# Kernel tuning notes

Measured on AMD Instinct MI355X. Metric: run time of the kernel, lower is better.

## Reference

```python
import jax, jax.numpy as jnp
import numpy as np

B, T, N = 64, 128, 64   # batch, win_size, input_size (= node_num)
H, E, K, CS = 64, 128, 7, 8  # hidden_size, embed_size, kernel_size, control_size
NEG_SLOPE = 0.2


def _p(key, shape, scale=0.05):
    return scale * jax.random.normal(key, shape, dtype=jnp.float32)


def setup_inputs() -> dict:
    key = jax.random.key(0)
    ks = jax.random.split(key, 32)
    inp = {
        "x": jax.random.normal(ks[0], (B, T, N), dtype=jnp.float32),
        "y": jax.random.normal(ks[1], (B, T, CS), dtype=jnp.float32),
        # Conv1d(N -> N, kernel K)
        "conv_w": _p(ks[2], (N, N, K)),
        "conv_b": _p(ks[3], (N,)),
        # rnn_enc GRU: input N -> hidden H
        "We_ih": _p(ks[4], (3 * H, N)), "We_hh": _p(ks[5], (3 * H, H)),
        "be_ih": _p(ks[6], (3 * H,)), "be_hh": _p(ks[7], (3 * H,)),
        # MP_GAT linears
        "Ww": _p(ks[8], (E, 2 * T)), "bw": _p(ks[9], (E,)),
        "Wa": _p(ks[10], (1, E)), "ba": _p(ks[11], (1,)),
        # encoder GRU: input H+N -> H
        "Wm_ih": _p(ks[12], (3 * H, H + N)), "Wm_hh": _p(ks[13], (3 * H, H)),
        "bm_ih": _p(ks[14], (3 * H,)), "bm_hh": _p(ks[15], (3 * H,)),
        # rnn_dec GRU: input H -> H
        "Wd_ih": _p(ks[16], (3 * H, H)), "Wd_hh": _p(ks[17], (3 * H, H)),
        "bd_ih": _p(ks[18], (3 * H,)), "bd_hh": _p(ks[19], (3 * H,)),
        # fc_dec: H -> N
        "W_dec": _p(ks[20], (N, H)), "b_dec": _p(ks[21], (N,)),
        # fc_pred: Linear(H,N), ReLU, Linear(N,N)
        "W_p1": _p(ks[22], (N, H)), "b_p1": _p(ks[23], (N,)),
        "W_p2": _p(ks[24], (N, N)), "b_p2": _p(ks[25], (N,)),
    }
    return inp


def gru_seq(x_seq, Wih, Whh, bih, bhh):
    """torch nn.GRU (batch_first, h0=0). x_seq: [B,T,in] -> [B,T,H]."""
    gi = jnp.einsum('bti,gi->btg', x_seq, Wih) + bih  # [B,T,3H] (precompute input proj)
    h0 = jnp.zeros((x_seq.shape[0], Whh.shape[1]), x_seq.dtype)

    def step(h, gi_t):
        gh = h @ Whh.T + bhh
        i_r, i_z, i_n = jnp.split(gi_t, 3, axis=-1)
        h_r, h_z, h_n = jnp.split(gh, 3, axis=-1)
        r = jax.nn.sigmoid(i_r + h_r)
        z = jax.nn.sigmoid(i_z + h_z)
        n = jnp.tanh(i_n + r * h_n)
        h_new = (1.0 - z) * n + z * h
        return h_new, h_new

    _, hs = jax.lax.scan(step, h0, jnp.swapaxes(gi, 0, 1))
    return jnp.swapaxes(hs, 0, 1)


def _forward(x, y, conv_w, conv_b, We_ih, We_hh, be_ih, be_hh, Ww, bw, Wa, ba,
             Wm_ih, Wm_hh, bm_ih, bm_hh, Wd_ih, Wd_hh, bd_ih, bd_hh,
             W_dec, b_dec, W_p1, b_p1, W_p2, b_p2):
    # ---- CNN: pad 'same' + Conv1d + SELU. x: [B,T,N] -> channels first [B,N,T]
    pad = (K - 1) // 2
    xc = jnp.swapaxes(x, 1, 2)
    c = jax.lax.conv_general_dilated(xc, conv_w, (1,), [(pad, pad)],
                                     dimension_numbers=('NCH', 'OIH', 'NCH'))
    c = jax.nn.selu(c + conv_b[None, :, None])  # [B,N,T]
    c_btn = jnp.swapaxes(c, 1, 2)               # [B,T,N]

    # ---- rnn_enc GRU over time
    h_out = gru_seq(c_btn, We_ih, We_hh, be_ih, be_hh)  # [B,T,H]

    # ---- MP_GAT on c (v: [B, node, seq] = [B,N,T])
    v = c
    vi = jnp.broadcast_to(v[:, :, None, :], (B, N, N, T))
    vj = jnp.broadcast_to(v[:, None, :, :], (B, N, N, T))
    v_cat = jnp.concatenate([vi, vj], axis=-1)          # [B,N,N,2T]
    x_w = jax.nn.leaky_relu(jnp.einsum('bijt,et->bije', v_cat, Ww) + bw, NEG_SLOPE)
    e = (jnp.einsum('bije,oe->bijo', x_w, Wa) + ba)[..., 0]  # [B,N,N]
    attention = jax.nn.softmax(e, axis=2)
    # dropout is identity in eval mode
    h_mp = jax.nn.sigmoid(jnp.einsum('bij,bjt->bit', attention, v))  # [B,N,T]
    h_mp = jnp.swapaxes(h_mp, 1, 2)                      # [B,T,N]

    # ---- encoder / decoder GRUs (dropout = identity in eval)
    h_cat = jnp.concatenate([h_out, h_mp], axis=2)       # [B,T,H+N]
    h_enc = gru_seq(h_cat, Wm_ih, Wm_hh, bm_ih, bm_hh)
    h_dec = gru_seq(h_enc, Wd_ih, Wd_hh, bd_ih, bd_hh)

    recon = h_dec @ W_dec.T + b_dec                      # [B,T,N]
    p = jax.nn.relu(h_dec[:, 0, :] @ W_p1.T + b_p1)
    pred = p @ W_p2.T + b_p2                             # [B,N]
    return recon, pred


def reference(x, y, conv_w, conv_b, We_ih, We_hh, be_ih, be_hh, Ww, bw, Wa, ba,
              Wm_ih, Wm_hh, bm_ih, bm_hh, Wd_ih, Wd_hh, bd_ih, bd_hh,
              W_dec, b_dec, W_p1, b_p1, W_p2, b_p2):
    return _forward(x, y, conv_w, conv_b, We_ih, We_hh, be_ih, be_hh, Ww, bw, Wa, ba,
                    Wm_ih, Wm_hh, bm_ih, bm_hh, Wd_ih, Wd_hh, bd_ih, bd_hh,
                    W_dec, b_dec, W_p1, b_p1, W_p2, b_p2)
```

## Files before the change

### kernel.cpp

```cpp
#include <hip/hip_runtime.h>
#include <math.h>

#define BB 64
#define TT 128
#define NN 64
#define HH 64
#define EE 128
#define KK 7
#define GG 192

typedef _Float16 half2_t __attribute__((ext_vector_type(2)));

__device__ __forceinline__ float sigmoidf_(float x){ return 1.f/(1.f+expf(-x)); }
__device__ __forceinline__ float fsig_(float x){
  return __builtin_amdgcn_rcpf(1.f + __builtin_amdgcn_exp2f(-1.44269504f * x));
}
__device__ __forceinline__ float ftanh_(float x){
  return fmaf(-2.f, __builtin_amdgcn_rcpf(1.f + __builtin_amdgcn_exp2f(2.88539008f * x)), 1.f);
}

#define PIPE_BARRIER() asm volatile("s_waitcnt lgkmcnt(0)\ns_barrier" ::: "memory")
#define LGKM0() asm volatile("s_waitcnt lgkmcnt(0)" ::: "memory")

__device__ __forceinline__ void loadrow_(float* d, const float* src){
  const float4* p = (const float4*)src;
  #pragma unroll
  for (int i = 0; i < 16; ++i) {
    float4 v = p[i];
    d[4*i] = v.x; d[4*i+1] = v.y; d[4*i+2] = v.z; d[4*i+3] = v.w;
  }
}
__device__ __forceinline__ void loadroww_(half2_t* d, const float* src){
  const float4* p = (const float4*)src;
  #pragma unroll
  for (int i = 0; i < 16; ++i) {
    float4 v = p[i];
    d[2*i]   = half2_t{(_Float16)v.x, (_Float16)v.y};
    d[2*i+1] = half2_t{(_Float16)v.z, (_Float16)v.w};
  }
}
__device__ __forceinline__ void load_h16_(const _Float16* hs, half2_t* hp){
  const float4* s4 = (const float4*)hs;
  #pragma unroll
  for (int j = 0; j < 8; ++j) {
    float4 v = s4[j];
    const half2_t* q = (const half2_t*)&v;
    hp[4*j] = q[0]; hp[4*j+1] = q[1]; hp[4*j+2] = q[2]; hp[4*j+3] = q[3];
  }
}
__device__ __forceinline__ void mvdot3_(const half2_t* hp, const half2_t* w0,
                                        const half2_t* w1, const half2_t* w2,
                                        float& a0, float& a1, float& a2){
  #pragma unroll
  for (int i = 0; i < 32; ++i) {
    a0 = __builtin_amdgcn_fdot2(hp[i], w0[i], a0, false);
    a1 = __builtin_amdgcn_fdot2(hp[i], w1[i], a1, false);
    a2 = __builtin_amdgcn_fdot2(hp[i], w2[i], a2, false);
  }
}

__global__ void conv_s12_kernel(const float* __restrict__ x, const float* __restrict__ w,
                                const float* __restrict__ bias, const float* __restrict__ Ww,
                                float* __restrict__ c_nt, float* __restrict__ c_btn,
                                float* __restrict__ s1, float* __restrict__ s2) {
  const int og = blockIdx.x, b = blockIdx.y, t = threadIdx.x;
  const int o0 = og * 8;
  __shared__ __align__(16) float xs[NN][TT + 1];
  __shared__ __align__(16) float ws[NN * KK][8];
  __shared__ __align__(16) float cs[8][TT];
  for (int idx = t; idx < TT * NN; idx += 128) {
    int tt = idx >> 6, nn = idx & 63;
    xs[nn][tt] = x[(size_t)(b * TT + tt) * NN + nn];
  }
  for (int idx = t; idx < NN * KK * 8; idx += 128) {
    int oo = idx & 7, ik = idx >> 3;
    ws[ik][oo] = w[(size_t)(o0 + oo) * (NN * KK) + ik];
  }
  __syncthreads();
  float acc[8];
  #pragma unroll
  for (int oo = 0; oo < 8; ++oo) acc[oo] = bias[o0 + oo];
  for (int i = 0; i < NN; ++i) {
    #pragma unroll
    for (int k = 0; k < KK; ++k) {
      int tt = t + k - 3;
      if (tt >= 0 && tt < TT) {
        float xv = xs[i][tt];
        const float* wp = &ws[i * KK + k][0];
        float4 w0 = *(const float4*)wp;
        float4 w1 = *(const float4*)(wp + 4);
        acc[0] += xv * w0.x; acc[1] += xv * w0.y; acc[2] += xv * w0.z; acc[3] += xv * w0.w;
        acc[4] += xv * w1.x; acc[5] += xv * w1.y; acc[6] += xv * w1.z; acc[7] += xv * w1.w;
      }
    }
  }
  const float alpha = 1.6732632423543772f, scale = 1.0507009873554805f;
  #pragma unroll
  for (int oo = 0; oo < 8; ++oo) {
    float a = acc[oo];
    float r = a > 0.f ? scale * a : scale * alpha * expm1f(a);
    int o = o0 + oo;
    c_nt[((size_t)b * NN + o) * TT + t] = r;
    c_btn[((size_t)b * TT + t) * NN + o] = r;
    cs[oo][t] = r;
  }
  __syncthreads();
  const float* w1 = Ww + (size_t)t * (2 * TT);
  const float* w2 = w1 + TT;
  float a1[8], a2l[8];
  #pragma unroll
  for (int r = 0; r < 8; ++r) { a1[r] = 0.f; a2l[r] = 0.f; }
  #pragma unroll 2
  for (int k = 0; k < TT; k += 4) {
    float4 wv1 = *(const float4*)(w1 + k);
    float4 wv2 = *(const float4*)(w2 + k);
    #pragma unroll
    for (int r = 0; r < 8; ++r) {
      float4 cv = *(const float4*)&cs[r][k];
      a1[r]  += cv.x * wv1.x + cv.y * wv1.y + cv.z * wv1.z + cv.w * wv1.w;
      a2l[r] += cv.x * wv2.x + cv.y * wv2.y + cv.z * wv2.z + cv.w * wv2.w;
    }
  }
  #pragma unroll
  for (int r = 0; r < 8; ++r) {
    s1[((size_t)b * NN + o0 + r) * EE + t] = a1[r];
    s2[((size_t)b * NN + o0 + r) * EE + t] = a2l[r];
  }
}

__global__ __launch_bounds__(512)
void gat_kernel(const float* __restrict__ s1, const float* __restrict__ s2,
                const float* __restrict__ bw, const float* __restrict__ Wa,
                const float* __restrict__ ba, const float* __restrict__ c_nt,
                float* __restrict__ hmp) {
  const int it = blockIdx.x, b = blockIdx.y, tid = threadIdx.x;
  const int i0 = it * 16;
  __shared__ float s2s[NN][EE + 1];
  __shared__ float s1b[16][EE];
  __shared__ float cs[NN][TT + 1];
  __shared__ float was[EE];
  __shared__ float att[16][NN + 1];
  for (int idx = tid; idx < NN * EE; idx += 512) {
    int j = idx >> 7, e = idx & 127;
    s2s[j][e] = s2[((size_t)b * NN + j) * EE + e] + bw[e];
  }
  for (int idx = tid; idx < 16 * EE; idx += 512) {
    int r = idx >> 7, e = idx & 127;
    s1b[r][e] = s1[((size_t)b * NN + i0 + r) * EE + e];
  }
  for (int idx = tid; idx < NN * TT; idx += 512) {
    int j = idx >> 7, t = idx & 127;
    cs[j][t] = c_nt[((size_t)b * NN + j) * TT + t];
  }
  if (tid < EE) was[tid] = Wa[tid];
  __syncthreads();
  const int wv = tid >> 6, j = tid & 63;
  #pragma unroll
  for (int pass = 0; pass < 2; ++pass) {
    const int il = pass * 8 + wv;
    float acc = 0.f;
    #pragma unroll 8
    for (int e = 0; e < EE; ++e) {
      float v = s1b[il][e] + s2s[j][e];
      v = v > 0.f ? v : 0.2f * v;
      acc += was[e] * v;
    }
    float ej = acc + ba[0];
    float mx = ej;
    for (int off = 32; off >= 1; off >>= 1) mx = fmaxf(mx, __shfl_xor(mx, off));
    float ex = __builtin_amdgcn_exp2f(1.44269504f * (ej - mx));
    float sm = ex;
    for (int off = 32; off >= 1; off >>= 1) sm += __shfl_xor(sm, off);
    att[il][j] = ex / sm;
  }
  __syncthreads();
  for (int o = tid; o < 16 * TT; o += 512) {
    int il = o & 15, t = o >> 4;
    float acc = 0.f;
    #pragma unroll 8
    for (int jj = 0; jj < NN; ++jj) acc += att[il][jj] * cs[jj][t];
    hmp[((size_t)b * TT + t) * NN + i0 + il] = sigmoidf_(acc);
  }
}

__global__ __launch_bounds__(512, 1)
void fused_chain8(const float* __restrict__ c_btn, const float* __restrict__ hmp,
                  const float* __restrict__ We_ih, const float* __restrict__ be_ih,
                  const float* __restrict__ We_hh, const float* __restrict__ be_hh,
                  const float* __restrict__ Wm_ih, const float* __restrict__ bm_ih,
                  const float* __restrict__ Wm_hh, const float* __restrict__ bm_hh,
                  const float* __restrict__ Wd_ih, const float* __restrict__ bd_ih,
                  const float* __restrict__ Wd_hh, const float* __restrict__ bd_hh,
                  const float* __restrict__ W_dec, const float* __restrict__ b_dec,
                  const float* __restrict__ W_p1, const float* __restrict__ b_p1,
                  const float* __restrict__ W_p2, const float* __restrict__ b_p2,
                  float* __restrict__ recon, float* __restrict__ pred) {
  const int b = blockIdx.x, tid = threadIdx.x, wid = tid >> 6, g = tid & 63;
  __shared__ __align__(16) _Float16 cbuf[2][HH], mbuf[2][HH];
  __shared__ __align__(16) _Float16 h1h[2][HH], h2h[2][HH], h3h[2][HH];
  __shared__ __align__(16) float h3f[2][HH];
  __shared__ __align__(16) float q1[2][GG], q2a[2][GG], q2b[2][GG], q3[2][GG];
  __shared__ __align__(16) float h0s[HH], ps[HH];

  half2_t wa[32], wb[32], wc[32];
  float wdec[64];
  float b0 = 0.f, b1 = 0.f, b2 = 0.f;
  float e0 = 0.f, e1 = 0.f, e2 = 0.f;
  if (wid == 0) {
    loadroww_(wa, We_hh + (size_t)g * HH);
    loadroww_(wb, We_hh + (size_t)(g + 64) * HH);
    loadroww_(wc, We_hh + (size_t)(g + 128) * HH);
    b0 = be_hh[g]; b1 = be_hh[64 + g]; b2 = be_hh[128 + g];
  } else if (wid == 1) {
    loadroww_(wa, Wm_hh + (size_t)g * HH);
    loadroww_(wb, Wm_hh + (size_t)(g + 64) * HH);
    loadroww_(wc, Wm_hh + (size_t)(g + 128) * HH);
    b0 = bm_hh[g]; b1 = bm_hh[64 + g]; b2 = bm_hh[128 + g];
  } else if (wid == 2) {
    loadroww_(wa, Wd_hh + (size_t)g * HH);
    loadroww_(wb, Wd_hh + (size_t)(g + 64) * HH);
    loadroww_(wc, Wd_hh + (size_t)(g + 128) * HH);
    b0 = bd_hh[g]; b1 = bd_hh[64 + g]; b2 = bd_hh[128 + g];
    e0 = bd_ih[g]; e1 = bd_ih[64 + g]; e2 = bd_ih[128 + g];
  } else if (wid == 3) {
    loadrow_(wdec, W_dec + (size_t)g * HH);
    b0 = b_dec[g];
  } else if (wid == 4) {
    loadroww_(wa, Wm_ih + (size_t)g * 128);
    loadroww_(wb, Wm_ih + (size_t)(g + 64) * 128);
    loadroww_(wc, Wm_ih + (size_t)(g + 128) * 128);
  } else if (wid == 5) {
    loadroww_(wa, Wd_ih + (size_t)g * HH);
    loadroww_(wb, Wd_ih + (size_t)(g + 64) * HH);
    loadroww_(wc, Wd_ih + (size_t)(g + 128) * HH);
  } else if (wid == 6) {
    loadroww_(wa, We_ih + (size_t)g * HH);
    loadroww_(wb, We_ih + (size_t)(g + 64) * HH);
    loadroww_(wc, We_ih + (size_t)(g + 128) * HH);
    b0 = be_ih[g]; b1 = be_ih[64 + g]; b2 = be_ih[128 + g];
  } else {
    loadroww_(wa, Wm_ih + (size_t)g * 128 + 64);
    loadroww_(wb, Wm_ih + (size_t)(g + 64) * 128 + 64);
    loadroww_(wc, Wm_ih + (size_t)(g + 128) * 128 + 64);
    b0 = bm_ih[g]; b1 = bm_ih[64 + g]; b2 = bm_ih[128 + g];
  }

  if (wid == 0) {
    h1h[0][g] = (_Float16)0.f; h1h[1][g] = (_Float16)0.f;
    h2h[0][g] = (_Float16)0.f; h2h[1][g] = (_Float16)0.f;
    h3h[0][g] = (_Float16)0.f; h3h[1][g] = (_Float16)0.f;
  }
  const float* cb = c_btn + (size_t)b * TT * NN + g;
  const float* hm = hmp   + (size_t)b * TT * NN + g;
  float pf0 = 0.f, pf1 = 0.f;
  if (wid == 6) {
    cbuf[0][g] = (_Float16)cb[0]; cbuf[1][g] = (_Float16)cb[NN];
    pf0 = cb[2 * NN]; pf1 = cb[3 * NN];
  }
  if (wid == 7) {
    mbuf[0][g] = (_Float16)hm[0]; mbuf[1][g] = (_Float16)hm[NN];
    pf0 = hm[2 * NN]; pf1 = hm[3 * NN];
  }
  if (wid <= 2) __builtin_amdgcn_s_setprio(1);
  __syncthreads();

  float hown = 0.f;
  for (int ph = 0; ph < TT + 6; ++ph) {
    const int pw = ph & 1, pr = pw ^ 1;
    if (wid == 6) {
      int t = ph;
      if (t < TT) {
        half2_t hp[32]; load_h16_(&cbuf[pw][0], hp);
        if (t + 2 < TT) cbuf[pw][g] = (_Float16)(pw ? pf1 : pf0);
        float a0 = b0, a1 = b1, a2 = b2;
        if (t + 4 < TT) { float nv = cb[(size_t)(t + 4) * NN]; if (pw) pf1 = nv; else pf0 = nv; }
        mvdot3_(hp, wa, wb, wc, a0, a1, a2);
        q1[pw][g] = a0; q1[pw][64 + g] = a1; q1[pw][128 + g] = a2;
      }
    } else if (wid == 0) {
      int t = ph - 1;
      if (t >= 0 && t < TT) {
        half2_t hp[32]; load_h16_(&h1h[pr][0], hp);
        float a0 = b0, a1 = b1, a2 = b2;
        mvdot3_(hp, wa, wb, wc, a0, a1, a2);
        float r = fsig_(q1[pr][g] + a0), z = fsig_(q1[pr][64 + g] + a1);
        float n = ftanh_(q1[pr][128 + g] + r * a2);
        hown = fmaf(z, hown - n, n);
        h1h[pw][g] = (_Float16)hown;
      }
    } else if (wid == 4) {
      int t = ph - 2;
      if (t >= 0 && t < TT) {
        half2_t hp[32]; load_h16_(&h1h[pr][0], hp);
        float a0 = 0.f, a1 = 0.f, a2 = 0.f;
        mvdot3_(hp, wa, wb, wc, a0, a1, a2);
        q2a[pw][g] = a0; q2a[pw][64 + g] = a1; q2a[pw][128 + g] = a2;
      }
    } else if (wid == 7) {
      int t = ph - 2;
      if (t >= 0 && t < TT) {
        half2_t hp[32]; load_h16_(&mbuf[pw][0], hp);
        if (t + 2 < TT) mbuf[pw][g] = (_Float16)(pw ? pf1 : pf0);
        float a0 = b0, a1 = b1, a2 = b2;
        if (t + 4 < TT) { float nv = hm[(size_t)(t + 4) * NN]; if (pw) pf1 = nv; else pf0 = nv; }
        mvdot3_(hp, wa, wb, wc, a0, a1, a2);
        q2b[pw][g] = a0; q2b[pw][64 + g] = a1; q2b[pw][128 + g] = a2;
      }
    } else if (wid == 1) {
      int t = ph - 3;
      if (t >= 0 && t < TT) {
        half2_t hp[32]; load_h16_(&h2h[pr][0], hp);
        float a0 = b0, a1 = b1, a2 = b2;
        mvdot3_(hp, wa, wb, wc, a0, a1, a2);
        float gr = q2a[pr][g] + q2b[pr][g];
        float gz = q2a[pr][64 + g] + q2b[pr][64 + g];
        float gn = q2a[pr][128 + g] + q2b[pr][128 + g];
        float r = fsig_(gr + a0), z = fsig_(gz + a1), n = ftanh_(gn + r * a2);
        hown = fmaf(z, hown - n, n);
        h2h[pw][g] = (_Float16)hown;
      }
    } else if (wid == 5) {
      int t = ph - 4;
      if (t >= 0 && t < TT) {
        half2_t hp[32]; load_h16_(&h2h[pr][0], hp);
        float a0 = 0.f, a1 = 0.f, a2 = 0.f;
        mvdot3_(hp, wa, wb, wc, a0, a1, a2);
        q3[pw][g] = a0; q3[pw][64 + g] = a1; q3[pw][128 + g] = a2;
      }
    } else if (wid == 2) {
      int t = ph - 5;
      if (t >= 0 && t < TT) {
        half2_t hp[32]; load_h16_(&h3h[pr][0], hp);
        float a0 = b0, a1 = b1, a2 = b2;
        mvdot3_(hp, wa, wb, wc, a0, a1, a2);
        float r = fsig_(q3[pr][g] + e0 + a0), z = fsig_(q3[pr][64 + g] + e1 + a1);
        float n = ftanh_(q3[pr][128 + g] + e2 + r * a2);
        hown = fmaf(z, hown - n, n);
        h3h[pw][g] = (_Float16)hown;
        h3f[pw][g] = hown;
        if (t == 0) h0s[g] = hown;
      }
    } else {
      int t = ph - 6;
      if (t >= 0) {
        const float4* h4 = (const float4*)&h3f[pr][0];
        float a0 = b0, a1 = 0.f;
        #pragma unroll
        for (int i = 0; i < 8; ++i) {
          float4 hv = h4[2 * i], hw = h4[2 * i + 1];
          a0 = fmaf(hv.x, wdec[8*i],   fmaf(hv.y, wdec[8*i+1], fmaf(hv.z, wdec[8*i+2], fmaf(hv.w, wdec[8*i+3], a0))));
          a1 = fmaf(hw.x, wdec[8*i+4], fmaf(hw.y, wdec[8*i+5], fmaf(hw.z, wdec[8*i+6], fmaf(hw.w, wdec[8*i+7], a1))));
        }
        recon[((size_t)b * TT + t) * NN + g] = a0 + a1;
      }
    }
    PIPE_BARRIER();
  }

  if (wid == 0) {
    float w1r[64]; loadrow_(w1r, W_p1 + (size_t)g * HH);
    const float4* h4 = (const float4*)&h0s[0];
    float a = b_p1[g];
    #pragma unroll
    for (int i = 0; i < 16; ++i) {
      float4 hv = h4[i];
      a = fmaf(hv.x, w1r[4*i], fmaf(hv.y, w1r[4*i+1], fmaf(hv.z, w1r[4*i+2], fmaf(hv.w, w1r[4*i+3], a))));
    }
    ps[g] = fmaxf(a, 0.f);
    LGKM0();
    float w2r[64]; loadrow_(w2r, W_p2 + (size_t)g * HH);
    const float4* p4 = (const float4*)&ps[0];
    float c2 = b_p2[g];
    #pragma unroll
    for (int i = 0; i < 16; ++i) {
      float4 pv = p4[i];
      c2 = fmaf(pv.x, w2r[4*i], fmaf(pv.y, w2r[4*i+1], fmaf(pv.z, w2r[4*i+2], fmaf(pv.w, w2r[4*i+3], c2))));
    }
    pred[(size_t)b * NN + g] = c2;
  }
}

extern "C" void kernel_launch(void* const* d_in, const int* in_sizes, int n_in,
                              void* d_out, int out_size, void* d_ws, size_t ws_size,
                              hipStream_t stream) {
  const float* x      = (const float*)d_in[0];
  const float* conv_w = (const float*)d_in[2];
  const float* conv_b = (const float*)d_in[3];
  const float* We_ih  = (const float*)d_in[4];
  const float* We_hh  = (const float*)d_in[5];
  const float* be_ih  = (const float*)d_in[6];
  const float* be_hh  = (const float*)d_in[7];
  const float* Ww     = (const float*)d_in[8];
  const float* bw     = (const float*)d_in[9];
  const float* Wa     = (const float*)d_in[10];
  const float* ba     = (const float*)d_in[11];
  const float* Wm_ih  = (const float*)d_in[12];
  const float* Wm_hh  = (const float*)d_in[13];
  const float* bm_ih  = (const float*)d_in[14];
  const float* bm_hh  = (const float*)d_in[15];
  const float* Wd_ih  = (const float*)d_in[16];
  const float* Wd_hh  = (const float*)d_in[17];
  const float* bd_ih  = (const float*)d_in[18];
  const float* bd_hh  = (const float*)d_in[19];
  const float* W_dec  = (const float*)d_in[20];
  const float* b_dec  = (const float*)d_in[21];
  const float* W_p1   = (const float*)d_in[22];
  const float* b_p1   = (const float*)d_in[23];
  const float* W_p2   = (const float*)d_in[24];
  const float* b_p2   = (const float*)d_in[25];
  float* out = (float*)d_out;

  float* wsf   = (float*)d_ws;
  float* c_nt  = wsf;
  float* c_btn = c_nt  + 524288;
  float* s1    = c_btn + 524288;
  float* s2    = s1    + 524288;
  float* hmp   = s2    + 524288;

  conv_s12_kernel<<<dim3(8, BB), 128, 0, stream>>>(x, conv_w, conv_b, Ww,
                                                   c_nt, c_btn, s1, s2);
  gat_kernel<<<dim3(4, BB), 512, 0, stream>>>(s1, s2, bw, Wa, ba, c_nt, hmp);
  fused_chain8<<<BB, 512, 0, stream>>>(c_btn, hmp,
                                       We_ih, be_ih, We_hh, be_hh,
                                       Wm_ih, bm_ih, Wm_hh, bm_hh,
                                       Wd_ih, bd_ih, Wd_hh, bd_hh,
                                       W_dec, b_dec, W_p1, b_p1, W_p2, b_p2,
                                       out, out + BB * TT * NN);
}
```

Before: 177.6 us.

## Replace per-phase block barrier with point-to-point LDS flag synchronization between wavefronts

Removes the block-wide barrier that ends every pipeline phase of the fused GRU chain. Each wavefront now publishes its progress in a shared-memory flag and spins only on the specific producer and consumer flags it depends on, so stages can drift without waiting for the slowest wave. This trades barrier stalls for spin-polling with s_sleep and relies on volatile LDS ordering for correctness, which adds race risk if a dependency is missed.

New measurement: 185.4 us. 1.04x slower.

```diff
diff --git a/kernel.cpp b/kernel.cpp
--- a/kernel.cpp
+++ b/kernel.cpp
@@ -19,8 +19,16 @@
   return fmaf(-2.f, __builtin_amdgcn_rcpf(1.f + __builtin_amdgcn_exp2f(2.88539008f * x)), 1.f);
 }
 
-#define PIPE_BARRIER() asm volatile("s_waitcnt lgkmcnt(0)\ns_barrier" ::: "memory")
 #define LGKM0() asm volatile("s_waitcnt lgkmcnt(0)" ::: "memory")
+
+__device__ __forceinline__ void wait_flag_(volatile int* f, int v){
+  while (*f < v) { __builtin_amdgcn_s_sleep(1); }
+  asm volatile("s_waitcnt lgkmcnt(0)" ::: "memory");
+}
+__device__ __forceinline__ void set_flag_(volatile int* f, int v, int lane){
+  asm volatile("s_waitcnt lgkmcnt(0)" ::: "memory");
+  if (lane == 0) *f = v;
+}
 
 __device__ __forceinline__ void loadrow_(float* d, const float* src){
   const float4* p = (const float4*)src;
@@ -184,23 +192,27 @@
 }
 
 __global__ __launch_bounds__(512, 1)
-void fused_chain8(const float* __restrict__ c_btn, const float* __restrict__ hmp,
-                  const float* __restrict__ We_ih, const float* __restrict__ be_ih,
-                  const float* __restrict__ We_hh, const float* __restrict__ be_hh,
-                  const float* __restrict__ Wm_ih, const float* __restrict__ bm_ih,
-                  const float* __restrict__ Wm_hh, const float* __restrict__ bm_hh,
-                  const float* __restrict__ Wd_ih, const float* __restrict__ bd_ih,
-                  const float* __restrict__ Wd_hh, const float* __restrict__ bd_hh,
-                  const float* __restrict__ W_dec, const float* __restrict__ b_dec,
-                  const float* __restrict__ W_p1, const float* __restrict__ b_p1,
-                  const float* __restrict__ W_p2, const float* __restrict__ b_p2,
-                  float* __restrict__ recon, float* __restrict__ pred) {
+void fused_chain8a(const float* __restrict__ c_btn, const float* __restrict__ hmp,
+                   const float* __restrict__ We_ih, const float* __restrict__ be_ih,
+                   const float* __restrict__ We_hh, const float* __restrict__ be_hh,
+                   const float* __restrict__ Wm_ih, const float* __restrict__ bm_ih,
+                   const float* __restrict__ Wm_hh, const float* __restrict__ bm_hh,
+                   const float* __restrict__ Wd_ih, const float* __restrict__ bd_ih,
+                   const float* __restrict__ Wd_hh, const float* __restrict__ bd_hh,
+                   const float* __restrict__ W_dec, const float* __restrict__ b_dec,
+                   const float* __restrict__ W_p1, const float* __restrict__ b_p1,
+                   const float* __restrict__ W_p2, const float* __restrict__ b_p2,
+                   float* __restrict__ recon, float* __restrict__ pred) {
   const int b = blockIdx.x, tid = threadIdx.x, wid = tid >> 6, g = tid & 63;
   __shared__ __align__(16) _Float16 cbuf[2][HH], mbuf[2][HH];
   __shared__ __align__(16) _Float16 h1h[2][HH], h2h[2][HH], h3h[2][HH];
   __shared__ __align__(16) float h3f[2][HH];
   __shared__ __align__(16) float q1[2][GG], q2a[2][GG], q2b[2][GG], q3[2][GG];
   __shared__ __align__(16) float h0s[HH], ps[HH];
+  __shared__ int flg[8];
+  volatile int* vf = (volatile int*)flg;
+
+  if (tid < 8) flg[tid] = -1;
 
   half2_t wa[32], wb[32], wc[32];
   float wdec[64];
@@ -265,7 +277,8 @@
   __syncthreads();
 
   float hown = 0.f;
-  for (int ph = 0; ph < TT + 6; ++ph) {
+  const int NPH = TT + 6;
+  for (int ph = 0; ph < NPH; ++ph) {
     const int pw = ph & 1, pr = pw ^ 1;
     if (wid == 6) {
       int t = ph;
@@ -275,25 +288,30 @@
         float a0 = b0, a1 = b1, a2 = b2;
         if (t + 4 < TT) { float nv = cb[(size_t)(t + 4) * NN]; if (pw) pf1 = nv; else pf0 = nv; }
         mvdot3_(hp, wa, wb, wc, a0, a1, a2);
+        wait_flag_(vf + 0, ph - 1);
         q1[pw][g] = a0; q1[pw][64 + g] = a1; q1[pw][128 + g] = a2;
       }
     } else if (wid == 0) {
       int t = ph - 1;
       if (t >= 0 && t < TT) {
+        wait_flag_(vf + 6, ph - 1);
         half2_t hp[32]; load_h16_(&h1h[pr][0], hp);
         float a0 = b0, a1 = b1, a2 = b2;
         mvdot3_(hp, wa, wb, wc, a0, a1, a2);
         float r = fsig_(q1[pr][g] + a0), z = fsig_(q1[pr][64 + g] + a1);
         float n = ftanh_(q1[pr][128 + g] + r * a2);
         hown = fmaf(z, hown - n, n);
+        wait_flag_(vf + 4, ph - 1);
         h1h[pw][g] = (_Float16)hown;
       }
     } else if (wid == 4) {
       int t = ph - 2;
       if (t >= 0 && t < TT) {
+        wait_flag_(vf + 0, ph - 1);
         half2_t hp[32]; load_h16_(&h1h[pr][0], hp);
         float a0 = 0.f, a1 = 0.f, a2 = 0.f;
         mvdot3_(hp, wa, wb, wc, a0, a1, a2);
+        wait_flag_(vf + 1, ph - 1);
         q2a[pw][g] = a0; q2a[pw][64 + g] = a1; q2a[pw][128 + g] = a2;
       }
     } else if (wid == 7) {
@@ -304,11 +322,14 @@
         float a0 = b0, a1 = b1, a2 = b2;
         if (t + 4 < TT) { float nv = hm[(size_t)(t + 4) * NN]; if (pw) pf1 = nv; else pf0 = nv; }
         mvdot3_(hp, wa, wb, wc, a0, a1, a2);
+        wait_flag_(vf + 1, ph - 1);
         q2b[pw][g] = a0; q2b[pw][64 + g] = a1; q2b[pw][128 + g] = a2;
       }
     } else if (wid == 1) {
       int t = ph - 3;
       if (t >= 0 && t < TT) {
+        wait_flag_(vf + 4, ph - 1);
+        wait_flag_(vf + 7, ph - 1);
         half2_t hp[32]; load_h16_(&h2h[pr][0], hp);
         float a0 = b0, a1 = b1, a2 = b2;
         mvdot3_(hp, wa, wb, wc, a0, a1, a2);
@@ -317,19 +338,23 @@
         float gn = q2a[pr][128 + g] + q2b[pr][128 + g];
         float r = fsig_(gr + a0), z = fsig_(gz + a1), n = ftanh_(gn + r * a2);
         hown = fmaf(z, hown - n, n);
+        wait_flag_(vf + 5, ph - 1);
         h2h[pw][g] = (_Float16)hown;
       }
     } else if (wid == 5) {
       int t = ph - 4;
       if (t >= 0 && t < TT) {
+        wait_flag_(vf + 1, ph - 1);
         half2_t hp[32]; load_h16_(&h2h[pr][0], hp);
         float a0 = 0.f, a1 = 0.f, a2 = 0.f;
         mvdot3_(hp, wa, wb, wc, a0, a1, a2);
+        wait_flag_(vf + 2, ph - 1);
         q3[pw][g] = a0; q3[pw][64 + g] = a1; q3[pw][128 + g] = a2;
       }
     } else if (wid == 2) {
       int t = ph - 5;
       if (t >= 0 && t < TT) {
+        wait_flag_(vf + 5, ph - 1);
         half2_t hp[32]; load_h16_(&h3h[pr][0], hp);
         float a0 = b0, a1 = b1, a2 = b2;
         mvdot3_(hp, wa, wb, wc, a0, a1, a2);
@@ -337,12 +362,14 @@
         float n = ftanh_(q3[pr][128 + g] + e2 + r * a2);
         hown = fmaf(z, hown - n, n);
         h3h[pw][g] = (_Float16)hown;
+        wait_flag_(vf + 3, ph - 1);
         h3f[pw][g] = hown;
         if (t == 0) h0s[g] = hown;
       }
     } else {
       int t = ph - 6;
       if (t >= 0) {
+        wait_flag_(vf + 2, ph - 1);
         const float4* h4 = (const float4*)&h3f[pr][0];
         float a0 = b0, a1 = 0.f;
         #pragma unroll
@@ -354,10 +381,11 @@
         recon[((size_t)b * TT + t) * NN + g] = a0 + a1;
       }
     }
-    PIPE_BARRIER();
+    set_flag_(vf + wid, ph, g);
   }
 
   if (wid == 0) {
+    wait_flag_(vf + 2, 5);
     float w1r[64]; loadrow_(w1r, W_p1 + (size_t)g * HH);
     const float4* h4 = (const float4*)&h0s[0];
     float a = b_p1[g];
@@ -420,10 +448,10 @@
   conv_s12_kernel<<<dim3(8, BB), 128, 0, stream>>>(x, conv_w, conv_b, Ww,
                                                    c_nt, c_btn, s1, s2);
   gat_kernel<<<dim3(4, BB), 512, 0, stream>>>(s1, s2, bw, Wa, ba, c_nt, hmp);
-  fused_chain8<<<BB, 512, 0, stream>>>(c_btn, hmp,
-                                       We_ih, be_ih, We_hh, be_hh,
-                                       Wm_ih, bm_ih, Wm_hh, bm_hh,
-                                       Wd_ih, bd_ih, Wd_hh, bd_hh,
-                                       W_dec, b_dec, W_p1, b_p1, W_p2, b_p2,
-                                       out, out + BB * TT * NN);
-}
+  fused_chain8a<<<BB, 512, 0, stream>>>(c_btn, hmp,
+                                        We_ih, be_ih, We_hh, be_hh,
+                                        Wm_ih, bm_ih, Wm_hh, bm_hh,
+                                        Wd_ih, bd_ih, Wd_hh, bd_hh,
+                                        W_dec, b_dec, W_p1, b_p1, W_p2, b_p2,
+                                        out, out + BB * TT * NN);
+}
```

## Fuse conv and GAT attention kernels, recomputing conv per block

Applied to the files above, without the earlier changes.

Merges the conv+projection kernel and the GAT kernel into one launch. Each of the 4 row-blocks per batch recomputes the full 64-channel conv and s2 projection in shared memory instead of round-tripping c_nt, s1 and s2 through global memory. This removes one launch and the intermediate global traffic, but the conv and s2 work is done four times per batch, and the per-block conv now uses 512 threads with smaller per-thread tiles.

Result: slower. 368.3 us (+107.4%).

```diff
diff --git a/kernel.cpp b/kernel.cpp
--- a/kernel.cpp
+++ b/kernel.cpp
@@ -59,102 +59,104 @@
   }
 }
 
-__global__ void conv_s12_kernel(const float* __restrict__ x, const float* __restrict__ w,
-                                const float* __restrict__ bias, const float* __restrict__ Ww,
-                                float* __restrict__ c_nt, float* __restrict__ c_btn,
-                                float* __restrict__ s1, float* __restrict__ s2) {
-  const int og = blockIdx.x, b = blockIdx.y, t = threadIdx.x;
-  const int o0 = og * 8;
-  __shared__ __align__(16) float xs[NN][TT + 1];
-  __shared__ __align__(16) float ws[NN * KK][8];
-  __shared__ __align__(16) float cs[8][TT];
-  for (int idx = t; idx < TT * NN; idx += 128) {
+__global__ __launch_bounds__(512)
+void conv_gat_kernel(const float* __restrict__ x, const float* __restrict__ w,
+                     const float* __restrict__ bias, const float* __restrict__ Ww,
+                     const float* __restrict__ bw, const float* __restrict__ Wa,
+                     const float* __restrict__ ba,
+                     float* __restrict__ c_btn, float* __restrict__ hmp) {
+  const int it = blockIdx.x, b = blockIdx.y, tid = threadIdx.x;
+  const int i0 = it * 16;
+  __shared__ __align__(16) float poolA[NN * 129];
+  __shared__ __align__(16) float cs[NN][132];
+  __shared__ __align__(16) char poolC[NN * KK * 16 * 4];
+  float (*xs)[129]  = (float(*)[129])poolA;
+  float (*s2s)[129] = (float(*)[129])poolA;
+  float (*ws)[16]   = (float(*)[16])poolC;
+  float (*s1b)[EE]  = (float(*)[EE])poolC;
+  float (*att)[NN + 1] = (float(*)[NN + 1])(poolC + 8192);
+  float* was = (float*)(poolC + 8192 + 4160);
+
+  for (int idx = tid; idx < TT * NN; idx += 512) {
     int tt = idx >> 6, nn = idx & 63;
     xs[nn][tt] = x[(size_t)(b * TT + tt) * NN + nn];
   }
-  for (int idx = t; idx < NN * KK * 8; idx += 128) {
-    int oo = idx & 7, ik = idx >> 3;
-    ws[ik][oo] = w[(size_t)(o0 + oo) * (NN * KK) + ik];
-  }
   __syncthreads();
-  float acc[8];
-  #pragma unroll
-  for (int oo = 0; oo < 8; ++oo) acc[oo] = bias[o0 + oo];
-  for (int i = 0; i < NN; ++i) {
+
+  const int t = tid & 127, cg = tid >> 7;
+  for (int ch0 = 0; ch0 < NN; ch0 += 16) {
+    for (int idx = tid; idx < NN * KK * 16; idx += 512) {
+      int oo = idx & 15, ik = idx >> 4;
+      ws[ik][oo] = w[(size_t)(ch0 + oo) * (NN * KK) + ik];
+    }
+    __syncthreads();
+    float acc[4];
     #pragma unroll
-    for (int k = 0; k < KK; ++k) {
-      int tt = t + k - 3;
-      if (tt >= 0 && tt < TT) {
-        float xv = xs[i][tt];
-        const float* wp = &ws[i * KK + k][0];
-        float4 w0 = *(const float4*)wp;
-        float4 w1 = *(const float4*)(wp + 4);
-        acc[0] += xv * w0.x; acc[1] += xv * w0.y; acc[2] += xv * w0.z; acc[3] += xv * w0.w;
-        acc[4] += xv * w1.x; acc[5] += xv * w1.y; acc[6] += xv * w1.z; acc[7] += xv * w1.w;
-      }
-    }
-  }
-  const float alpha = 1.6732632423543772f, scale = 1.0507009873554805f;
-  #pragma unroll
-  for (int oo = 0; oo < 8; ++oo) {
-    float a = acc[oo];
-    float r = a > 0.f ? scale * a : scale * alpha * expm1f(a);
-    int o = o0 + oo;
-    c_nt[((size_t)b * NN + o) * TT + t] = r;
-    c_btn[((size_t)b * TT + t) * NN + o] = r;
-    cs[oo][t] = r;
+    for (int j = 0; j < 4; ++j) acc[j] = bias[ch0 + cg * 4 + j];
+    for (int i = 0; i < NN; ++i) {
+      #pragma unroll
+      for (int k = 0; k < KK; ++k) {
+        int tt = t + k - 3;
+        if (tt >= 0 && tt < TT) {
+          float xv = xs[i][tt];
+          float4 w4 = *(const float4*)&ws[i * KK + k][cg * 4];
+          acc[0] += xv * w4.x; acc[1] += xv * w4.y; acc[2] += xv * w4.z; acc[3] += xv * w4.w;
+        }
+      }
+    }
+    const float alpha = 1.6732632423543772f, scale = 1.0507009873554805f;
+    #pragma unroll
+    for (int j = 0; j < 4; ++j) {
+      int o = ch0 + cg * 4 + j;
+      float a = acc[j];
+      float r = a > 0.f ? scale * a : scale * alpha * expm1f(a);
+      cs[o][t] = r;
+      if (it == 0) c_btn[((size_t)b * TT + t) * NN + o] = r;
+    }
+    __syncthreads();
+  }
+
+  {
+    const int e = tid & 127, grp = tid >> 7;
+    const float* w2r = Ww + (size_t)e * (2 * TT) + TT;
+    float bwv = bw[e];
+    #pragma unroll 2
+    for (int m = 0; m < 16; ++m) {
+      int j = grp * 16 + m;
+      float a0 = 0.f, a1 = 0.f;
+      #pragma unroll 4
+      for (int k = 0; k < TT; k += 8) {
+        float4 c0 = *(const float4*)&cs[j][k];
+        float4 c1 = *(const float4*)&cs[j][k + 4];
+        float4 v0 = *(const float4*)(w2r + k);
+        float4 v1 = *(const float4*)(w2r + k + 4);
+        a0 += c0.x * v0.x + c0.y * v0.y + c0.z * v0.z + c0.w * v0.w;
+        a1 += c1.x * v1.x + c1.y * v1.y + c1.z * v1.z + c1.w * v1.w;
+      }
+      s2s[j][e] = a0 + a1 + bwv;
+    }
+    const float* w1r = Ww + (size_t)e * (2 * TT);
+    #pragma unroll
+    for (int m = 0; m < 4; ++m) {
+      int r = grp * 4 + m;
+      float a0 = 0.f, a1 = 0.f;
+      #pragma unroll 4
+      for (int k = 0; k < TT; k += 8) {
+        float4 c0 = *(const float4*)&cs[i0 + r][k];
+        float4 c1 = *(const float4*)&cs[i0 + r][k + 4];
+        float4 v0 = *(const float4*)(w1r + k);
+        float4 v1 = *(const float4*)(w1r + k + 4);
+        a0 += c0.x * v0.x + c0.y * v0.y + c0.z * v0.z + c0.w * v0.w;
+        a1 += c1.x * v1.x + c1.y * v1.y + c1.z * v1.z + c1.w * v1.w;
+      }
+      s1b[r][e] = a0 + a1;
+    }
+    if (tid < EE) was[tid] = Wa[tid];
   }
   __syncthreads();
-  const float* w1 = Ww + (size_t)t * (2 * TT);
-  const float* w2 = w1 + TT;
-  float a1[8], a2l[8];
-  #pragma unroll
-  for (int r = 0; r < 8; ++r) { a1[r] = 0.f; a2l[r] = 0.f; }
-  #pragma unroll 2
-  for (int k = 0; k < TT; k += 4) {
-    float4 wv1 = *(const float4*)(w1 + k);
-    float4 wv2 = *(const float4*)(w2 + k);
-    #pragma unroll
-    for (int r = 0; r < 8; ++r) {
-      float4 cv = *(const float4*)&cs[r][k];
-      a1[r]  += cv.x * wv1.x + cv.y * wv1.y + cv.z * wv1.z + cv.w * wv1.w;
-      a2l[r] += cv.x * wv2.x + cv.y * wv2.y + cv.z * wv2.z + cv.w * wv2.w;
-    }
-  }
-  #pragma unroll
-  for (int r = 0; r < 8; ++r) {
-    s1[((size_t)b * NN + o0 + r) * EE + t] = a1[r];
-    s2[((size_t)b * NN + o0 + r) * EE + t] = a2l[r];
-  }
-}
-
-__global__ __launch_bounds__(512)
-void gat_kernel(const float* __restrict__ s1, const float* __restrict__ s2,
-                const float* __restrict__ bw, const float* __restrict__ Wa,
-                const float* __restrict__ ba, const float* __restrict__ c_nt,
-                float* __restrict__ hmp) {
-  const int it = blockIdx.x, b = blockIdx.y, tid = threadIdx.x;
-  const int i0 = it * 16;
-  __shared__ float s2s[NN][EE + 1];
-  __shared__ float s1b[16][EE];
-  __shared__ float cs[NN][TT + 1];
-  __shared__ float was[EE];
-  __shared__ float att[16][NN + 1];
-  for (int idx = tid; idx < NN * EE; idx += 512) {
-    int j = idx >> 7, e = idx & 127;
-    s2s[j][e] = s2[((size_t)b * NN + j) * EE + e] + bw[e];
-  }
-  for (int idx = tid; idx < 16 * EE; idx += 512) {
-    int r = idx >> 7, e = idx & 127;
-    s1b[r][e] = s1[((size_t)b * NN + i0 + r) * EE + e];
-  }
-  for (int idx = tid; idx < NN * TT; idx += 512) {
-    int j = idx >> 7, t = idx & 127;
-    cs[j][t] = c_nt[((size_t)b * NN + j) * TT + t];
-  }
-  if (tid < EE) was[tid] = Wa[tid];
-  __syncthreads();
+
   const int wv = tid >> 6, j = tid & 63;
+  const float ba0 = ba[0];
   #pragma unroll
   for (int pass = 0; pass < 2; ++pass) {
     const int il = pass * 8 + wv;
@@ -165,7 +167,7 @@
       v = v > 0.f ? v : 0.2f * v;
       acc += was[e] * v;
     }
-    float ej = acc + ba[0];
+    float ej = acc + ba0;
     float mx = ej;
     for (int off = 32; off >= 1; off >>= 1) mx = fmaxf(mx, __shfl_xor(mx, off));
     float ex = __builtin_amdgcn_exp2f(1.44269504f * (ej - mx));
@@ -174,12 +176,13 @@
     att[il][j] = ex / sm;
   }
   __syncthreads();
+
   for (int o = tid; o < 16 * TT; o += 512) {
-    int il = o & 15, t = o >> 4;
+    int il = o & 15, tt = o >> 4;
     float acc = 0.f;
     #pragma unroll 8
-    for (int jj = 0; jj < NN; ++jj) acc += att[il][jj] * cs[jj][t];
-    hmp[((size_t)b * TT + t) * NN + i0 + il] = sigmoidf_(acc);
+    for (int jj = 0; jj < NN; ++jj) acc += att[il][jj] * cs[jj][tt];
+    hmp[((size_t)b * TT + tt) * NN + i0 + il] = sigmoidf_(acc);
   }
 }
 
@@ -411,15 +414,11 @@
   float* out = (float*)d_out;
 
   float* wsf   = (float*)d_ws;
-  float* c_nt  = wsf;
-  float* c_btn = c_nt  + 524288;
-  float* s1    = c_btn + 524288;
-  float* s2    = s1    + 524288;
-  float* hmp   = s2    + 524288;
-
-  conv_s12_kernel<<<dim3(8, BB), 128, 0, stream>>>(x, conv_w, conv_b, Ww,
-                                                   c_nt, c_btn, s1, s2);
-  gat_kernel<<<dim3(4, BB), 512, 0, stream>>>(s1, s2, bw, Wa, ba, c_nt, hmp);
+  float* c_btn = wsf;
+  float* hmp   = c_btn + 524288;
+
+  conv_gat_kernel<<<dim3(4, BB), 512, 0, stream>>>(x, conv_w, conv_b, Ww, bw, Wa, ba,
+                                                   c_btn, hmp);
   fused_chain8<<<BB, 512, 0, stream>>>(c_btn, hmp,
                                        We_ih, be_ih, We_hh, be_hh,
                                        Wm_ih, bm_ih, Wm_hh, bm_hh,
```
